# Optimization experiments

Hardware: AMD Instinct MI355X
Metric: run time of the kernel (lower is better)

The kernel has to match this reference:

```python
import jax, jax.numpy as jnp
import numpy as np

N_CODEBOOKS = 4
N_EMBED = 1024
EMBED_DIM = 64
PATCH = 4
BETA = 0.25
EPS = 1e-5
USAGE_W = 0.01


def setup_inputs() -> dict:
    key = jax.random.key(0)
    k1, k2 = jax.random.split(key)
    z = jax.random.normal(k1, (8, 64, 128, 128), dtype=jnp.float32)
    # one EMA codebook per quantizer, initialized ~ randn like torch buffer
    codebooks = jax.random.normal(k2, (N_CODEBOOKS, N_EMBED, EMBED_DIM), dtype=jnp.float32)
    return {"z": z, "codebooks": codebooks}


def _usage_loss(indices, n_embed):
    # negative-entropy penalty on code usage (no gradient path: counts are ints)
    counts = jnp.bincount(indices.reshape(-1), length=n_embed).astype(jnp.float32)
    probs = (counts + EPS) / (counts.sum() + EPS * n_embed)
    entropy = -jnp.sum(probs * jnp.log(probs + EPS))
    return jnp.log(jnp.float32(n_embed)) - entropy


def _ema_quantize(residual, embedding):
    # residual: [N, C, ph, pw], embedding: [n_e, C]; eval mode (no EMA buffer update)
    N, C, ph, pw = residual.shape
    z_flat = residual.transpose(0, 2, 3, 1).reshape(-1, C)  # [M, C]
    d = (jnp.sum(z_flat ** 2, axis=1, keepdims=True)
         + jnp.sum(embedding ** 2, axis=1)
         - 2.0 * z_flat @ embedding.T)  # [M, n_e]
    idx = jnp.argmin(d, axis=1)  # [M]
    z_q = embedding[idx].reshape(N, ph, pw, C).transpose(0, 3, 1, 2)  # [N, C, ph, pw]
    loss = BETA * jnp.mean((jax.lax.stop_gradient(z_q) - residual) ** 2)
    z_q_st = residual + jax.lax.stop_gradient(z_q - residual)  # straight-through
    return z_q_st, loss, idx.reshape(N, ph, pw)


def reference(z, codebooks):
    B, C, H, W = z.shape
    h, w = H // PATCH, W // PATCH
    # b c (h ph) (w pw) -> (b h w) c ph pw
    zp = (z.reshape(B, C, h, PATCH, w, PATCH)
            .transpose(0, 2, 4, 1, 3, 5)
            .reshape(B * h * w, C, PATCH, PATCH))
    zq_acc = jnp.zeros_like(zp)
    residual = zp
    losses, all_idx = [], []
    for i in range(N_CODEBOOKS):
        zq_i, loss_i, idx_i = _ema_quantize(residual, codebooks[i])
        loss_i = loss_i + USAGE_W * _usage_loss(idx_i, N_EMBED)
        zq_acc = zq_acc + zq_i
        residual = residual - zq_i
        losses.append(loss_i)
        all_idx.append(idx_i.reshape(idx_i.shape[0], -1))  # [N, ph*pw]
    loss = jnp.stack(losses).sum()
    # (b h w) c ph pw -> b c (h ph) (w pw)
    z_q = (zq_acc.reshape(B, h, w, C, PATCH, PATCH)
                 .transpose(0, 3, 1, 4, 2, 5)
                 .reshape(B, C, H, W))
    # [N, patch_area, n_codebooks] -> [b, h, w, patch_area, n_codebooks]
    min_idx = jnp.stack(all_idx, axis=-1).reshape(B, h, w, PATCH * PATCH, N_CODEBOOKS)
    return z_q, loss, min_idx
```

## Files before the change

### kernel.cpp

```cpp
#include <hip/hip_runtime.h>
#include <math.h>

typedef __attribute__((ext_vector_type(8))) short short8;
typedef __attribute__((ext_vector_type(4))) float f32x4;

#define NCB 4
#define NE 1024
#define DIM 64
#define HW 16384
#define NPIX 131072
#define NWAVES 4096
#define MSE_DENOM 8388608.0f
#define EPSF 1e-5f
#define CH1_BYTES 16384
#define NCH1 8
#define CAP 1024

__device__ __forceinline__ unsigned short f2bf(float x) {
    unsigned u = __float_as_uint(x);
    u += 0x7fffu + ((u >> 16) & 1u);
    return (unsigned short)(u >> 16);
}
__device__ __forceinline__ float bf2f(unsigned short h) {
    return __uint_as_float(((unsigned)h) << 16);
}

__global__ __launch_bounds__(64) void rvq_norms(const float* __restrict__ cb,
                                                float* __restrict__ nrmh,
                                                float* __restrict__ emax2) {
    int code = blockIdx.x * 64 + threadIdx.x;
    const float4* row = reinterpret_cast<const float4*>(cb + (size_t)code * DIM);
    float s0 = 0.f, s1 = 0.f, s2 = 0.f, s3 = 0.f;
#pragma unroll
    for (int k = 0; k < 16; ++k) {
        float4 v = row[k];
        s0 = fmaf(v.x, v.x, s0); s1 = fmaf(v.y, v.y, s1);
        s2 = fmaf(v.z, v.z, s2); s3 = fmaf(v.w, v.w, s3);
    }
    float n2 = (s0 + s1) + (s2 + s3);
    nrmh[code] = -0.5f * n2;
    atomicMax((int*)&emax2[blockIdx.x >> 4], __float_as_int(n2));
}

__global__ __launch_bounds__(256) void rvq_presplit(const float* __restrict__ cb,
                                                    unsigned short* __restrict__ gB1,
                                                    unsigned short* __restrict__ gBf) {
    int blk = blockIdx.x;
    int tid = threadIdx.x;
    int code64 = tid >> 2, dg = tid & 3;
    int c0 = (blk & 15) << 6;
    int i  = blk >> 4;
    int C  = c0 + code64;
    const float4* s4 = reinterpret_cast<const float4*>(
        cb + ((size_t)i * NE + C) * DIM + dg * 16);
    float v[16];
    {
        float4 q;
        q = s4[0]; v[0]=q.x; v[1]=q.y; v[2]=q.z; v[3]=q.w;
        q = s4[1]; v[4]=q.x; v[5]=q.y; v[6]=q.z; v[7]=q.w;
        q = s4[2]; v[8]=q.x; v[9]=q.y; v[10]=q.z; v[11]=q.w;
        q = s4[3]; v[12]=q.x; v[13]=q.y; v[14]=q.z; v[15]=q.w;
    }
    char* out1 = reinterpret_cast<char*>(gB1) + (size_t)i * 131072 + (size_t)C * 128;
    char* outf = reinterpret_cast<char*>(gBf) + (size_t)i * 393216 + (size_t)C * 384;
    int sw = (C & 7) << 4;
#pragma unroll
    for (int h = 0; h < 2; ++h) {
        short8 p1, p2, p3;
#pragma unroll
        for (int e = 0; e < 8; ++e) {
            float t = v[h * 8 + e];
            unsigned short u1 = f2bf(t); t -= bf2f(u1);
            unsigned short u2 = f2bf(t); t -= bf2f(u2);
            unsigned short u3 = f2bf(t);
            p1[e] = (short)u1; p2[e] = (short)u2; p3[e] = (short)u3;
        }
        int al = dg * 32 + h * 16;
        *reinterpret_cast<short8*>(out1 + (al ^ sw)) = p1;
        *reinterpret_cast<short8*>(outf + al)        = p1;
        *reinterpret_cast<short8*>(outf + 128 + al)  = p2;
        *reinterpret_cast<short8*>(outf + 256 + al)  = p3;
    }
}

__device__ __forceinline__ void gload16(const void* gsrc, void* ldst) {
    __builtin_amdgcn_global_load_lds(
        (const __attribute__((address_space(1))) unsigned int*)gsrc,
        (__attribute__((address_space(3))) unsigned int*)ldst, 16, 0, 0);
}

__global__ __launch_bounds__(256, 2) void rvq_main(
    const float* __restrict__ z, const unsigned short* __restrict__ gB1,
    const unsigned short* __restrict__ gBf,
    const float* __restrict__ nrmh, const float* __restrict__ emax2,
    const float* __restrict__ cb,
    float* __restrict__ out_zq, float* __restrict__ out_idx,
    unsigned* __restrict__ hist, float* __restrict__ msePartial)
{
    __shared__ uint4 sB[2][CH1_BYTES / 16];
    __shared__ int   sBest[4][32];
    __shared__ float sRn[4][32];
    __shared__ int   sList[4][CAP];
    __shared__ int   sCnt[4];

    const int tid  = threadIdx.x;
    const int lane = tid & 63;
    const int wid  = tid >> 6;
    const int col  = lane & 15;
    const int g    = lane >> 4;
    const int blockPix = blockIdx.x * 128;
    char* sBase = reinterpret_cast<char*>(sB);
    const int sw = (col & 7) << 4;
    const char* gB1b = reinterpret_cast<const char*>(gB1);
    const char* gBfb = reinterpret_cast<const char*>(gBf);

#pragma unroll
    for (int k = 0; k < 4; ++k)
        gload16(gB1b + k * 4096 + tid * 16, sBase + k * 4096 + tid * 16);

    size_t zb[2];
#pragma unroll
    for (int m = 0; m < 2; ++m) {
        int pf = blockPix + wid * 32 + m * 16 + col;
        zb[m] = (size_t)(pf >> 14) * 1048576 + (size_t)(pf & 16383);
    }

    float r[2][2][8];
#pragma unroll
    for (int m = 0; m < 2; ++m)
#pragma unroll
        for (int kh = 0; kh < 2; ++kh)
#pragma unroll
            for (int e = 0; e < 8; ++e)
                r[m][kh][e] = z[zb[m] + (size_t)(kh * 32 + g * 8 + e) * HW];

    for (int i = 0; i < NCB; ++i) {
        const char* gB1i = gB1b + (size_t)i * 131072;
        const char* gBfi = gBfb + (size_t)i * 393216;
        const float* nrm_i = nrmh + i * NE;
        if (lane == 0) sCnt[wid] = 0;

        short8 A[3][2][2];
        float rn2[2] = {0.f, 0.f};
#pragma unroll
        for (int m = 0; m < 2; ++m)
#pragma unroll
            for (int kh = 0; kh < 2; ++kh)
#pragma unroll
                for (int e = 0; e < 8; ++e) {
                    float t0 = r[m][kh][e];
                    rn2[m] = fmaf(t0, t0, rn2[m]);
                    float t = t0;
                    unsigned short u1 = f2bf(t); t -= bf2f(u1);
                    unsigned short u2 = f2bf(t); t -= bf2f(u2);
                    unsigned short u3 = f2bf(t);
                    A[0][m][kh][e] = (short)u1;
                    A[1][m][kh][e] = (short)u2;
                    A[2][m][kh][e] = (short)u3;
                }
#pragma unroll
        for (int m = 0; m < 2; ++m) {
            rn2[m] += __shfl_xor(rn2[m], 16, 64);
            rn2[m] += __shfl_xor(rn2[m], 32, 64);
        }
        if (lane < 16) { sRn[wid][lane] = rn2[0]; sRn[wid][16 + lane] = rn2[1]; }

        float maxv[2][4];
#pragma unroll
        for (int m = 0; m < 2; ++m)
#pragma unroll
            for (int rr = 0; rr < 4; ++rr) maxv[m][rr] = -3.4e38f;

        for (int c = 0; c < NCH1; ++c) {
            __syncthreads();
            {
                int nc = (c < NCH1 - 1) ? c + 1 : 0;
                const char* gc = gB1i + (size_t)nc * CH1_BYTES;
                char* sbn = sBase + ((c + 1) & 1) * CH1_BYTES;
#pragma unroll
                for (int k = 0; k < 4; ++k)
                    gload16(gc + k * 4096 + tid * 16, sbn + k * 4096 + tid * 16);
            }
            const char* sbc = sBase + (c & 1) * CH1_BYTES;
#pragma unroll
            for (int sub = 0; sub < 8; ++sub) {
                const int code = (sub << 4) + col;
                float nh = nrm_i[(c << 7) + code];
                short8 B0 = *reinterpret_cast<const short8*>(
                    sbc + ((((code << 7) + (g << 4))) ^ sw));
                short8 B1 = *reinterpret_cast<const short8*>(
                    sbc + ((((code << 7) + 64 + (g << 4))) ^ sw));
                f32x4 acc0, acc1;
#pragma unroll
                for (int rr = 0; rr < 4; ++rr) { acc0[rr] = nh; acc1[rr] = nh; }
                __builtin_amdgcn_s_setprio(1);
                acc0 = __builtin_amdgcn_mfma_f32_16x16x32_bf16(A[0][0][0], B0, acc0, 0, 0, 0);
                acc1 = __builtin_amdgcn_mfma_f32_16x16x32_bf16(A[0][1][0], B0, acc1, 0, 0, 0);
                acc0 = __builtin_amdgcn_mfma_f32_16x16x32_bf16(A[0][0][1], B1, acc0, 0, 0, 0);
                acc1 = __builtin_amdgcn_mfma_f32_16x16x32_bf16(A[0][1][1], B1, acc1, 0, 0, 0);
                __builtin_amdgcn_s_setprio(0);
#pragma unroll
                for (int rr = 0; rr < 4; ++rr) {
                    maxv[0][rr] = fmaxf(maxv[0][rr], acc0[rr]);
                    maxv[1][rr] = fmaxf(maxv[1][rr], acc1[rr]);
                }
            }
        }

#pragma unroll
        for (int m = 0; m < 2; ++m)
#pragma unroll
            for (int rr = 0; rr < 4; ++rr) {
#pragma unroll
                for (int off = 1; off < 16; off <<= 1)
                    maxv[m][rr] = fmaxf(maxv[m][rr], __shfl_xor(maxv[m][rr], off, 64));
            }

        float thr[2][4];
        {
            float en = sqrtf(emax2[i]);
#pragma unroll
            for (int m = 0; m < 2; ++m)
#pragma unroll
                for (int rr = 0; rr < 4; ++rr) {
                    float rn = sqrtf(sRn[wid][m * 16 + g * 4 + rr]);
                    thr[m][rr] = maxv[m][rr] - (0.0205f * rn * en + 8e-3f);
                }
        }

        for (int c = 0; c < NCH1; ++c) {
            __syncthreads();
            if (c < NCH1 - 1) {
                const char* gc = gB1i + (size_t)(c + 1) * CH1_BYTES;
                char* sbn = sBase + ((c + 1) & 1) * CH1_BYTES;
#pragma unroll
                for (int k = 0; k < 4; ++k)
                    gload16(gc + k * 4096 + tid * 16, sbn + k * 4096 + tid * 16);
            }
            const char* sbc = sBase + (c & 1) * CH1_BYTES;
#pragma unroll
            for (int sub = 0; sub < 8; ++sub) {
                const int code = (sub << 4) + col;
                float nh = nrm_i[(c << 7) + code];
                short8 B0 = *reinterpret_cast<const short8*>(
                    sbc + ((((code << 7) + (g << 4))) ^ sw));
                short8 B1 = *reinterpret_cast<const short8*>(
                    sbc + ((((code << 7) + 64 + (g << 4))) ^ sw));
                f32x4 acc0, acc1;
#pragma unroll
                for (int rr = 0; rr < 4; ++rr) { acc0[rr] = nh; acc1[rr] = nh; }
                __builtin_amdgcn_s_setprio(1);
                acc0 = __builtin_amdgcn_mfma_f32_16x16x32_bf16(A[0][0][0], B0, acc0, 0, 0, 0);
                acc1 = __builtin_amdgcn_mfma_f32_16x16x32_bf16(A[0][1][0], B0, acc1, 0, 0, 0);
                acc0 = __builtin_amdgcn_mfma_f32_16x16x32_bf16(A[0][0][1], B1, acc0, 0, 0, 0);
                acc1 = __builtin_amdgcn_mfma_f32_16x16x32_bf16(A[0][1][1], B1, acc1, 0, 0, 0);
                __builtin_amdgcn_s_setprio(0);
                bool anyhit = false;
#pragma unroll
                for (int rr = 0; rr < 4; ++rr) {
                    anyhit |= (acc0[rr] >= thr[0][rr]);
                    anyhit |= (acc1[rr] >= thr[1][rr]);
                }
                unsigned long long mb = __ballot(anyhit);
                if (mb) {
                    unsigned long long colmask = 0x0001000100010001ULL << col;
                    bool push = anyhit &&
                        !(mb & colmask & ((lane == 0) ? 0ULL : ((1ULL << lane) - 1)));
                    if (push) {
                        int p = atomicAdd(&sCnt[wid], 1);
                        if (p < CAP) sList[wid][p] = (c << 7) + code;
                    }
                }
            }
        }

        if (i < NCB - 1) {
            const char* gn = gB1b + (size_t)(i + 1) * 131072;
#pragma unroll
            for (int k = 0; k < 4; ++k)
                gload16(gn + k * 4096 + tid * 16, sBase + k * 4096 + tid * 16);
        }

        float bestv[2][4]; int besti[2][4];
#pragma unroll
        for (int m = 0; m < 2; ++m)
#pragma unroll
            for (int rr = 0; rr < 4; ++rr) { bestv[m][rr] = -3.4e38f; besti[m][rr] = 0x7fffffff; }

        int ncand = sCnt[wid]; if (ncand > CAP) ncand = CAP;
        for (int b = 0; b < ncand; b += 16) {
            int ci = b + col;
            int code = sList[wid][ci < ncand ? ci : 0];
            const char* base = gBfi + (size_t)code * 384;
            short8 B[3][2];
#pragma unroll
            for (int s = 0; s < 3; ++s) {
                B[s][0] = *reinterpret_cast<const short8*>(base + s * 128 + (g << 4));
                B[s][1] = *reinterpret_cast<const short8*>(base + s * 128 + 64 + (g << 4));
            }
            float nh = nrm_i[code];
            f32x4 acc0, acc1;
#pragma unroll
            for (int rr = 0; rr < 4; ++rr) { acc0[rr] = nh; acc1[rr] = nh; }
            __builtin_amdgcn_s_setprio(1);
#pragma unroll
            for (int sb = 0; sb < 3; ++sb) {
#pragma unroll
                for (int sa = 0; sa < 3 - sb; ++sa) {
                    acc0 = __builtin_amdgcn_mfma_f32_16x16x32_bf16(A[sa][0][0], B[sb][0], acc0, 0, 0, 0);
                    acc1 = __builtin_amdgcn_mfma_f32_16x16x32_bf16(A[sa][1][0], B[sb][0], acc1, 0, 0, 0);
                    acc0 = __builtin_amdgcn_mfma_f32_16x16x32_bf16(A[sa][0][1], B[sb][1], acc0, 0, 0, 0);
                    acc1 = __builtin_amdgcn_mfma_f32_16x16x32_bf16(A[sa][1][1], B[sb][1], acc1, 0, 0, 0);
                }
            }
            __builtin_amdgcn_s_setprio(0);
#pragma unroll
            for (int rr = 0; rr < 4; ++rr) {
                float s0 = acc0[rr];
                if (s0 > bestv[0][rr] || (s0 == bestv[0][rr] && code < besti[0][rr])) {
                    bestv[0][rr] = s0; besti[0][rr] = code;
                }
                float s1 = acc1[rr];
                if (s1 > bestv[1][rr] || (s1 == bestv[1][rr] && code < besti[1][rr])) {
                    bestv[1][rr] = s1; besti[1][rr] = code;
                }
            }
        }

#pragma unroll
        for (int m = 0; m < 2; ++m)
#pragma unroll
            for (int rr = 0; rr < 4; ++rr) {
                float v = bestv[m][rr]; int ix = besti[m][rr];
#pragma unroll
                for (int off = 1; off < 16; off <<= 1) {
                    float ov = __shfl_xor(v, off, 64);
                    int   oi = __shfl_xor(ix, off, 64);
                    if (ov > v || (ov == v && oi < ix)) { v = ov; ix = oi; }
                }
                besti[m][rr] = ix;
            }
        if (col == 0) {
#pragma unroll
            for (int m = 0; m < 2; ++m)
#pragma unroll
                for (int rr = 0; rr < 4; ++rr)
                    sBest[wid][m * 16 + g * 4 + rr] = besti[m][rr];
        }

        const float* cbi = cb + (size_t)i * NE * DIM;
        if (lane < 16) {
#pragma unroll
            for (int m = 0; m < 2; ++m) {
                int pfr = blockPix + wid * 32 + m * 16 + lane;
                int bb = pfr >> 14, yy = (pfr >> 7) & 127, xx = pfr & 127;
                int bi = sBest[wid][m * 16 + lane];
                size_t off = (size_t)bb * 65536 + (size_t)(yy >> 2) * 2048
                           + (size_t)(xx >> 2) * 64
                           + (size_t)(((yy & 3) << 2) + (xx & 3)) * 4 + (size_t)i;
                out_idx[off] = (float)bi;
                atomicAdd(&hist[i * NE + bi], 1u);
            }
        }

#pragma unroll
        for (int m = 0; m < 2; ++m) {
            const int best = sBest[wid][m * 16 + col];
            const float* er = cbi + (size_t)best * DIM;
#pragma unroll
            for (int kh = 0; kh < 2; ++kh) {
                const float4* e4 = reinterpret_cast<const float4*>(er + kh * 32 + g * 8);
                float4 q0 = e4[0], q1 = e4[1];
                r[m][kh][0] -= q0.x; r[m][kh][1] -= q0.y;
                r[m][kh][2] -= q0.z; r[m][kh][3] -= q0.w;
                r[m][kh][4] -= q1.x; r[m][kh][5] -= q1.y;
                r[m][kh][6] -= q1.z; r[m][kh][7] -= q1.w;
            }
        }

        float s = 0.f;
#pragma unroll
        for (int m = 0; m < 2; ++m)
#pragma unroll
            for (int kh = 0; kh < 2; ++kh)
#pragma unroll
                for (int e = 0; e < 8; ++e) s = fmaf(r[m][kh][e], r[m][kh][e], s);
#pragma unroll
        for (int d_ = 32; d_ > 0; d_ >>= 1) s += __shfl_down(s, d_, 64);
        if (lane == 0) msePartial[i * NWAVES + blockIdx.x * 4 + wid] = s;
    }

#pragma unroll
    for (int m = 0; m < 2; ++m)
#pragma unroll
        for (int kh = 0; kh < 2; ++kh)
#pragma unroll
            for (int e = 0; e < 8; ++e) {
                size_t o = zb[m] + (size_t)(kh * 32 + g * 8 + e) * HW;
                out_zq[o] = z[o] - r[m][kh][e];
            }
}

__global__ __launch_bounds__(1024) void rvq_finalize(
    const unsigned* __restrict__ hist, const float* __restrict__ msePartial,
    float* __restrict__ out_loss)
{
    __shared__ float red[1024];
    int t = threadIdx.x;
    float loss = 0.f;
    for (int i = 0; i < NCB; ++i) {
        float cnt = (float)hist[i * NE + t];
        float prob = (cnt + EPSF) / (131072.0f + EPSF * 1024.0f);
        red[t] = -prob * logf(prob + EPSF);
        __syncthreads();
        for (int s = 512; s > 0; s >>= 1) { if (t < s) red[t] += red[t + s]; __syncthreads(); }
        float entropy = red[0];
        __syncthreads();
        float acc = 0.f;
#pragma unroll
        for (int k = 0; k < 4; ++k) acc += msePartial[i * NWAVES + k * 1024 + t];
        red[t] = acc;
        __syncthreads();
        for (int s = 512; s > 0; s >>= 1) { if (t < s) red[t] += red[t + s]; __syncthreads(); }
        float mse_sum = red[0];
        __syncthreads();
        loss += 0.25f * (mse_sum / MSE_DENOM) + 0.01f * (logf(1024.0f) - entropy);
    }
    if (t == 0) out_loss[0] = loss;
}

extern "C" void kernel_launch(void* const* d_in, const int* in_sizes, int n_in,
                              void* d_out, int out_size, void* d_ws, size_t ws_size,
                              hipStream_t stream) {
    const float* z  = (const float*)d_in[0];
    const float* cb = (const float*)d_in[1];

    float* out      = (float*)d_out;
    float* out_zq   = out;
    float* out_loss = out + 8388608;
    float* out_idx  = out + 8388609;

    unsigned* hist        = (unsigned*)d_ws;
    float*    emax2       = (float*)((char*)d_ws + 16384);
    float*    nrmh        = (float*)((char*)d_ws + 32768);
    float*    msePartial  = (float*)((char*)d_ws + 49152);
    unsigned short* gB1   = (unsigned short*)((char*)d_ws + 131072);
    unsigned short* gBf   = (unsigned short*)((char*)d_ws + 655360);

    hipMemsetAsync(d_ws, 0, 16448, stream);
    rvq_norms<<<64, 64, 0, stream>>>(cb, nrmh, emax2);
    rvq_presplit<<<64, 256, 0, stream>>>(cb, gB1, gBf);
    rvq_main<<<1024, 256, 0, stream>>>(z, gB1, gBf, nrmh, emax2, cb,
                                       out_zq, out_idx, hist, msePartial);
    rvq_finalize<<<1, 1024, 0, stream>>>(hist, msePartial, out_loss);
}
```

Baseline: 430.7 us.

## Fuse max-finding and candidate-filter passes into one single-pass running-max filter

Replaces the two-pass coarse search (first pass computes the exact per-row max score, second pass recomputes the bf16 MFMAs and collects codes within a margin of the max) with a single pass. Candidates are collected against a running max that is reduced across lanes after each chunk. This halves the first-stage MFMA work and codebook chunk loads. The cost is that the early running max is looser, so more candidates may be pushed to the list, raising the candidate count and the risk of overflowing CAP.

Measured after the change: 502.5 us. 1.17x slower.

```diff
diff --git a/kernel.cpp b/kernel.cpp
--- a/kernel.cpp
+++ b/kernel.cpp
@@ -165,6 +165,18 @@
         }
         if (lane < 16) { sRn[wid][lane] = rn2[0]; sRn[wid][16 + lane] = rn2[1]; }
 
+        float margin[2][4];
+        {
+            float en = sqrtf(emax2[i]);
+#pragma unroll
+            for (int m = 0; m < 2; ++m)
+#pragma unroll
+                for (int rr = 0; rr < 4; ++rr) {
+                    float rn = sqrtf(sRn[wid][m * 16 + g * 4 + rr]);
+                    margin[m][rr] = 0.0205f * rn * en + 8e-3f;
+                }
+        }
+
         float maxv[2][4];
 #pragma unroll
         for (int m = 0; m < 2; ++m)
@@ -173,9 +185,8 @@
 
         for (int c = 0; c < NCH1; ++c) {
             __syncthreads();
-            {
-                int nc = (c < NCH1 - 1) ? c + 1 : 0;
-                const char* gc = gB1i + (size_t)nc * CH1_BYTES;
+            if (c < NCH1 - 1) {
+                const char* gc = gB1i + (size_t)(c + 1) * CH1_BYTES;
                 char* sbn = sBase + ((c + 1) & 1) * CH1_BYTES;
 #pragma unroll
                 for (int k = 0; k < 4; ++k)
@@ -199,67 +210,13 @@
                 acc0 = __builtin_amdgcn_mfma_f32_16x16x32_bf16(A[0][0][1], B1, acc0, 0, 0, 0);
                 acc1 = __builtin_amdgcn_mfma_f32_16x16x32_bf16(A[0][1][1], B1, acc1, 0, 0, 0);
                 __builtin_amdgcn_s_setprio(0);
+                bool anyhit = false;
 #pragma unroll
                 for (int rr = 0; rr < 4; ++rr) {
                     maxv[0][rr] = fmaxf(maxv[0][rr], acc0[rr]);
                     maxv[1][rr] = fmaxf(maxv[1][rr], acc1[rr]);
-                }
-            }
-        }
-
-#pragma unroll
-        for (int m = 0; m < 2; ++m)
-#pragma unroll
-            for (int rr = 0; rr < 4; ++rr) {
-#pragma unroll
-                for (int off = 1; off < 16; off <<= 1)
-                    maxv[m][rr] = fmaxf(maxv[m][rr], __shfl_xor(maxv[m][rr], off, 64));
-            }
-
-        float thr[2][4];
-        {
-            float en = sqrtf(emax2[i]);
-#pragma unroll
-            for (int m = 0; m < 2; ++m)
-#pragma unroll
-                for (int rr = 0; rr < 4; ++rr) {
-                    float rn = sqrtf(sRn[wid][m * 16 + g * 4 + rr]);
-                    thr[m][rr] = maxv[m][rr] - (0.0205f * rn * en + 8e-3f);
-                }
-        }
-
-        for (int c = 0; c < NCH1; ++c) {
-            __syncthreads();
-            if (c < NCH1 - 1) {
-                const char* gc = gB1i + (size_t)(c + 1) * CH1_BYTES;
-                char* sbn = sBase + ((c + 1) & 1) * CH1_BYTES;
-#pragma unroll
-                for (int k = 0; k < 4; ++k)
-                    gload16(gc + k * 4096 + tid * 16, sbn + k * 4096 + tid * 16);
-            }
-            const char* sbc = sBase + (c & 1) * CH1_BYTES;
-#pragma unroll
-            for (int sub = 0; sub < 8; ++sub) {
-                const int code = (sub << 4) + col;
-                float nh = nrm_i[(c << 7) + code];
-                short8 B0 = *reinterpret_cast<const short8*>(
-                    sbc + ((((code << 7) + (g << 4))) ^ sw));
-                short8 B1 = *reinterpret_cast<const short8*>(
-                    sbc + ((((code << 7) + 64 + (g << 4))) ^ sw));
-                f32x4 acc0, acc1;
-#pragma unroll
-                for (int rr = 0; rr < 4; ++rr) { acc0[rr] = nh; acc1[rr] = nh; }
-                __builtin_amdgcn_s_setprio(1);
-                acc0 = __builtin_amdgcn_mfma_f32_16x16x32_bf16(A[0][0][0], B0, acc0, 0, 0, 0);
-                acc1 = __builtin_amdgcn_mfma_f32_16x16x32_bf16(A[0][1][0], B0, acc1, 0, 0, 0);
-                acc0 = __builtin_amdgcn_mfma_f32_16x16x32_bf16(A[0][0][1], B1, acc0, 0, 0, 0);
-                acc1 = __builtin_amdgcn_mfma_f32_16x16x32_bf16(A[0][1][1], B1, acc1, 0, 0, 0);
-                __builtin_amdgcn_s_setprio(0);
-                bool anyhit = false;
-#pragma unroll
-                for (int rr = 0; rr < 4; ++rr) {
-                    anyhit |= (acc0[rr] >= thr[0][rr]);
-                    anyhit |= (acc1[rr] >= thr[1][rr]);
+                    anyhit |= (acc0[rr] >= maxv[0][rr] - margin[0][rr]);
+                    anyhit |= (acc1[rr] >= maxv[1][rr] - margin[1][rr]);
                 }
                 unsigned long long mb = __ballot(anyhit);
                 if (mb) {
@@ -272,6 +229,14 @@
                     }
                 }
             }
+#pragma unroll
+            for (int m = 0; m < 2; ++m)
+#pragma unroll
+                for (int rr = 0; rr < 4; ++rr) {
+#pragma unroll
+                    for (int off = 1; off < 16; off <<= 1)
+                        maxv[m][rr] = fmaxf(maxv[m][rr], __shfl_xor(maxv[m][rr], off, 64));
+                }
         }
 
         if (i < NCB - 1) {
```
